# Kernel optimization log

Measured on AMD Instinct MI355X. Metric: run time of the kernel, lower is better.

## Reference

```python
import jax, jax.numpy as jnp
import numpy as np

H = 64          # hidden_size
IN = 6          # input_size
PREDICT = 10    # predict_size


def _lstm_cell(x_t, h, c, Wih, Whh, bih, bhh):
    # PyTorch gate order: i, f, g, o ; gates = x W_ih^T + b_ih + h W_hh^T + b_hh
    g = x_t @ Wih.T + bih + h @ Whh.T + bhh            # [B, 4H]
    i, f, gg, o = jnp.split(g, 4, axis=-1)
    c_new = jax.nn.sigmoid(f) * c + jax.nn.sigmoid(i) * jnp.tanh(gg)
    h_new = jax.nn.sigmoid(o) * jnp.tanh(c_new)
    return h_new, c_new


def setup_inputs() -> dict:
    key = jax.random.key(0)
    ks = jax.random.split(key, 12)
    B, T = 4096, 1024
    s = 1.0 / np.sqrt(H)  # torch default uniform init bound
    u = lambda k, shape: jax.random.uniform(k, shape, jnp.float32, -s, s)
    return {
        "x": jax.random.normal(ks[0], (B, T, IN), jnp.float32),
        "W_ih0": u(ks[1], (4 * H, IN)),
        "W_hh0": u(ks[2], (4 * H, H)),
        "b_ih0": u(ks[3], (4 * H,)),
        "b_hh0": u(ks[4], (4 * H,)),
        "W_ih1": u(ks[5], (4 * H, H)),
        "W_hh1": u(ks[6], (4 * H, H)),
        "b_ih1": u(ks[7], (4 * H,)),
        "b_hh1": u(ks[8], (4 * H,)),
        "fc_w": u(ks[9], (IN, H)),
        "fc_b": u(ks[10], (IN,)),
    }


def reference(x, W_ih0, W_hh0, b_ih0, b_hh0, W_ih1, W_hh1, b_ih1, b_hh1, fc_w, fc_b):
    B = x.shape[0]
    zeros = jnp.zeros((B, H), x.dtype)
    init = (zeros, zeros, zeros, zeros)  # h0, c0, h1, c1

    def stacked_step(carry, x_t):
        h0, c0, h1, c1 = carry
        h0, c0 = _lstm_cell(x_t, h0, c0, W_ih0, W_hh0, b_ih0, b_hh0)
        h1, c1 = _lstm_cell(h0, h1, c1, W_ih1, W_hh1, b_ih1, b_hh1)
        return (h0, c0, h1, c1), None

    # Encoder: scan over time (batch_first -> transpose to [T, B, IN])
    carry, _ = jax.lax.scan(stacked_step, init, jnp.swapaxes(x, 0, 1))

    def dec_step(state, _):
        dec_in, c = state
        c, _ = stacked_step(c, dec_in)
        pred = c[0 + 2] @ fc_w.T + fc_b  # top-layer h -> [B, IN]
        return (pred, c), pred

    dec_in0 = x[:, -1, :]
    _, preds = jax.lax.scan(dec_step, (dec_in0, carry), None, length=PREDICT)
    return jnp.swapaxes(preds, 0, 1)  # [B, PREDICT, IN]
```

## Files before the change

kernel.cpp:

```cpp
#include <hip/hip_runtime.h>

#define T_SEQ   1024
#define INDIM   6
#define HDIM    64
#define NPRED   10
#define CHNK    128
#define S0      104
#define NROWS   16

typedef __bf16         bf16x8 __attribute__((ext_vector_type(8)));
typedef float          f32x4  __attribute__((ext_vector_type(4)));
typedef unsigned short us4    __attribute__((ext_vector_type(4)));

#define MFMA16(a, b, c) __builtin_amdgcn_mfma_f32_16x16x32_bf16((a), (b), (c), 0, 0, 0)

static __device__ __forceinline__ float bf2f(unsigned short b) {
  union { unsigned int u; float f; } v; v.u = ((unsigned int)b) << 16; return v.f;
}
static __device__ __forceinline__ unsigned short f2bf(float f) {
  union { float f; unsigned int u; } v; v.f = f;
  unsigned int r = v.u + 0x7FFFu + ((v.u >> 16) & 1u);
  return (unsigned short)(r >> 16);
}

template <bool F32>
__global__ __launch_bounds__(512, 2)
void lstm2_pipe(const void* __restrict__ xv,
                const void* __restrict__ Wih0v,
                const void* __restrict__ Whh0v,
                const void* __restrict__ bih0v,
                const void* __restrict__ bhh0v,
                const void* __restrict__ Wih1v,
                const void* __restrict__ Whh1v,
                const void* __restrict__ bih1v,
                const void* __restrict__ bhh1v,
                const void* __restrict__ fcwv,
                const void* __restrict__ fcbv,
                void* __restrict__ outv)
{
  {
    const unsigned short* w0u = (const unsigned short*)Wih0v;
    int votes = 0;
#pragma unroll
    for (int i = 0; i < 16; ++i) {
      const unsigned e = (w0u[2 * i] >> 7) & 0xFF;
      votes += (e >= 0x80 || e <= 0x40) ? 1 : 0;
    }
    if ((votes >= 4) != F32) return;
  }

  __shared__ __align__(16) unsigned short A0[2][NROWS * S0];
  __shared__ __align__(16) unsigned short A1[2][NROWS * S0];
  __shared__ __align__(16) unsigned short XB[NROWS * CHNK * INDIM];
  __shared__ __align__(16) unsigned short FCW[INDIM * HDIM];
  __shared__ float FCB[INDIM];

  const int tid   = threadIdx.x;
  const int lane  = tid & 63;
  const int wave  = tid >> 6;
  const bool isA  = (wave < 4);
  const int  wv4  = wave & 3;
  const int  q    = lane >> 4;
  const int  n    = lane & 15;
  const int  u    = 16 * wv4 + n;
  const int rbase = blockIdx.x * NROWS;

  {
    unsigned short* p0 = &A0[0][0];
    unsigned short* p1 = &A1[0][0];
    for (int i = tid; i < 2 * NROWS * S0; i += 512) { p0[i] = 0; p1[i] = 0; }
  }
  for (int i = tid; i < INDIM * HDIM; i += 512) {
    if constexpr (F32) FCW[i] = f2bf(((const float*)fcwv)[i]);
    else               FCW[i] = ((const unsigned short*)fcwv)[i];
  }
  if (tid < INDIM) {
    if constexpr (F32) FCB[tid] = ((const float*)fcbv)[tid];
    else               FCB[tid] = bf2f(((const unsigned short*)fcbv)[tid]);
  }

  auto ld1 = [&](const void* p, int i) -> float {
    if constexpr (F32) return ((const float*)p)[i];
    else               return bf2f(((const unsigned short*)p)[i]);
  };
  auto ld8 = [&](const void* W, int off) -> bf16x8 {
    union { unsigned short us[8]; bf16x8 v; } t;
    if constexpr (F32) {
      const float* p = (const float*)W + off;
#pragma unroll
      for (int j = 0; j < 8; ++j) t.us[j] = f2bf(p[j]);
    } else {
      t.v = *(const bf16x8*)((const unsigned short*)W + off);
    }
    return t.v;
  };

  auto load_chunk = [&](int t0c) {
    if constexpr (F32) {
      const char* xb = (const char*)xv;
      for (int c = tid; c < NROWS * 192; c += 512) {
        const int row = c / 192;
        const int off = c - row * 192;
        const float4 v = *(const float4*)(xb + (size_t)(rbase + row) * (T_SEQ * INDIM * 4)
                                             + (size_t)t0c * (INDIM * 4) + (size_t)off * 16);
        us4 o;
        o.x = f2bf(v.x); o.y = f2bf(v.y); o.z = f2bf(v.z); o.w = f2bf(v.w);
        *(us4*)((char*)XB + (size_t)c * 8) = o;
      }
    } else {
      const char* xb = (const char*)xv;
      for (int c = tid; c < NROWS * 96; c += 512) {
        const int row = c / 96;
        const int off = c - row * 96;
        const int4 v = *(const int4*)(xb + (size_t)(rbase + row) * (T_SEQ * INDIM * 2)
                                         + (size_t)t0c * (INDIM * 2) + (size_t)off * 16);
        *(int4*)((char*)XB + (size_t)c * 16) = v;
      }
    }
  };

  load_chunk(0);
  __syncthreads();

  const int xrow   = tid / INDIM;
  const int xk     = tid - xrow * INDIM;
  const int xWrOff = xrow * S0 + HDIM + xk;
  const int xbBase = xrow * (CHNK * INDIM) + xk;

  if (tid < 96) A0[0][xWrOff] = XB[xbBase];
  __syncthreads();

  const int aOff  = n * S0 + 8 * q;
  const int hOffW = n * S0 + 16 * wv4 + 4 * q;
  const int bOff  = 16 * wv4 + 4 * q;

  float cc[4] = {0.f, 0.f, 0.f, 0.f};

  auto ldbias = [&](const void* b1, const void* b2, int gt) -> f32x4 {
    f32x4 r;
#pragma unroll
    for (int j = 0; j < 4; ++j)
      r[j] = ld1(b1, 64 * gt + bOff + j) + ld1(b2, 64 * gt + bOff + j);
    return r;
  };

  auto act4 = [&](const f32x4 gI, const f32x4 gF, const f32x4 gG, const f32x4 gO,
                  unsigned short* dst) {
    unsigned short hb[4];
#pragma unroll
    for (int r = 0; r < 4; ++r) {
      const float Ae = __builtin_amdgcn_exp2f(gF[r] * -1.442695040888963f);
      const float Be = __builtin_amdgcn_exp2f(gI[r] * -1.442695040888963f);
      const float Ge = __builtin_amdgcn_exp2f(gG[r] * -2.885390081777927f);
      const float M1 = (1.0f + Be) * (1.0f + Ge);
      const float nm = cc[r] * M1 + (1.0f - Ge) * (1.0f + Ae);
      cc[r] = nm * __builtin_amdgcn_rcpf((1.0f + Ae) * M1);
      const float Oe = __builtin_amdgcn_exp2f(gO[r] * -1.442695040888963f);
      const float Ee = __builtin_amdgcn_exp2f(cc[r] * -2.885390081777927f);
      hb[r] = f2bf((1.0f - Ee) * __builtin_amdgcn_rcpf((1.0f + Ee) * (1.0f + Oe)));
    }
    const unsigned int lo = (unsigned int)hb[0] | ((unsigned int)hb[1] << 16);
    const unsigned int hi = (unsigned int)hb[2] | ((unsigned int)hb[3] << 16);
    uint2 pk; pk.x = lo; pk.y = hi;
    *(uint2*)(dst + hOffW) = pk;
  };

  unsigned short* H0 = &A0[0][0];
  unsigned short* H1 = &A1[1][0];

  if (isA) {
    bf16x8 WA[12]; f32x4 bvA[4];
#pragma unroll
    for (int gt = 0; gt < 4; ++gt) {
      const int col = 64 * gt + u;
      WA[gt * 3 + 0] = ld8(Whh0v, col * HDIM + 8 * q);
      WA[gt * 3 + 1] = ld8(Whh0v, col * HDIM + 32 + 8 * q);
      union { unsigned short us[8]; bf16x8 v; } t2;
#pragma unroll
      for (int j = 0; j < 8; ++j) t2.us[j] = 0;
      if (q == 0) {
#pragma unroll
        for (int j = 0; j < INDIM; ++j) t2.us[j] = f2bf(ld1(Wih0v, col * INDIM + j));
      }
      WA[gt * 3 + 2] = t2.v;
      bvA[gt] = ldbias(bih0v, bhh0v, gt);
    }

    int t0v = 0;
    for (int i = 0; i <= T_SEQ; ++i) {
      if (((i + 1) & (CHNK - 1)) == 0 && (i + 1) < T_SEQ) {
        load_chunk(i + 1);
        __syncthreads();
        t0v = i + 1;
      }
      const int cur = i & 1;
      if (i < T_SEQ) {
        const unsigned short* A0c = &A0[cur][0];
        unsigned short*       A0n = &A0[cur ^ 1][0];
        const bf16x8 f0 = *(const bf16x8*)(A0c + aOff);
        const bf16x8 f1 = *(const bf16x8*)(A0c + aOff + 32);
        const bf16x8 f2 = *(const bf16x8*)(A0c + aOff + 64);
        f32x4 g0 = MFMA16(WA[0], f0, bvA[0]); g0 = MFMA16(WA[1],  f1, g0); g0 = MFMA16(WA[2],  f2, g0);
        f32x4 g1 = MFMA16(WA[3], f0, bvA[1]); g1 = MFMA16(WA[4],  f1, g1); g1 = MFMA16(WA[5],  f2, g1);
        f32x4 g2 = MFMA16(WA[6], f0, bvA[2]); g2 = MFMA16(WA[7],  f1, g2); g2 = MFMA16(WA[8],  f2, g2);
        f32x4 g3 = MFMA16(WA[9], f0, bvA[3]); g3 = MFMA16(WA[10], f1, g3); g3 = MFMA16(WA[11], f2, g3);
        act4(g0, g1, g2, g3, A0n);
        const int srct = (i + 1 < T_SEQ) ? (i + 1) : (T_SEQ - 1);
        if (tid < 96) A0n[xWrOff] = XB[xbBase + (srct - t0v) * INDIM];
      }
      __syncthreads();
    }
    for (int d = 0; d < NPRED; ++d) {
      const bf16x8 fa0 = *(const bf16x8*)(H0 + aOff);
      const bf16x8 fa1 = *(const bf16x8*)(H0 + aOff + 32);
      const bf16x8 fa2 = *(const bf16x8*)(H0 + aOff + 64);
      __syncthreads();
      {
        f32x4 g0 = MFMA16(WA[0], fa0, bvA[0]); g0 = MFMA16(WA[1],  fa1, g0); g0 = MFMA16(WA[2],  fa2, g0);
        f32x4 g1 = MFMA16(WA[3], fa0, bvA[1]); g1 = MFMA16(WA[4],  fa1, g1); g1 = MFMA16(WA[5],  fa2, g1);
        f32x4 g2 = MFMA16(WA[6], fa0, bvA[2]); g2 = MFMA16(WA[7],  fa1, g2); g2 = MFMA16(WA[8],  fa2, g2);
        f32x4 g3 = MFMA16(WA[9], fa0, bvA[3]); g3 = MFMA16(WA[10], fa1, g3); g3 = MFMA16(WA[11], fa2, g3);
        act4(g0, g1, g2, g3, H0);
      }
      __syncthreads();
      __syncthreads();
      if (tid < 96) {
        const unsigned short* h1row = H1 + xrow * S0;
        const int4* hp = (const int4*)h1row;
        const int4* wp = (const int4*)(&FCW[xk * HDIM]);
        float s = FCB[xk];
#pragma unroll
        for (int i8 = 0; i8 < 8; ++i8) {
          const int4 hv = hp[i8];
          const int4 wv2 = wp[i8];
          const unsigned int hu[4] = {(unsigned)hv.x, (unsigned)hv.y, (unsigned)hv.z, (unsigned)hv.w};
          const unsigned int wu[4] = {(unsigned)wv2.x, (unsigned)wv2.y, (unsigned)wv2.z, (unsigned)wv2.w};
#pragma unroll
          for (int k2 = 0; k2 < 4; ++k2) {
            union { unsigned int uu; float ff; } hl, hh2, wl, wh;
            hl.uu = hu[k2] << 16; hh2.uu = hu[k2] & 0xFFFF0000u;
            wl.uu = wu[k2] << 16; wh.uu  = wu[k2] & 0xFFFF0000u;
            s += hl.ff * wl.ff + hh2.ff * wh.ff;
          }
        }
        const unsigned short pb = f2bf(s);
        const size_t idx = (size_t)(rbase + xrow) * (NPRED * INDIM) + (size_t)d * INDIM + xk;
        if constexpr (F32) ((float*)outv)[idx] = s;
        else               ((unsigned short*)outv)[idx] = pb;
        H0[xWrOff] = pb;
      }
      __syncthreads();
    }
  } else {
    bf16x8 WB[16]; f32x4 bvB[4];
#pragma unroll
    for (int gt = 0; gt < 4; ++gt) {
      const int col = 64 * gt + u;
      WB[gt * 4 + 0] = ld8(Wih1v, col * HDIM + 8 * q);
      WB[gt * 4 + 1] = ld8(Wih1v, col * HDIM + 32 + 8 * q);
      WB[gt * 4 + 2] = ld8(Whh1v, col * HDIM + 8 * q);
      WB[gt * 4 + 3] = ld8(Whh1v, col * HDIM + 32 + 8 * q);
      bvB[gt] = ldbias(bih1v, bhh1v, gt);
    }

    for (int i = 0; i <= T_SEQ; ++i) {
      if (((i + 1) & (CHNK - 1)) == 0 && (i + 1) < T_SEQ) {
        load_chunk(i + 1);
        __syncthreads();
      }
      const int cur = i & 1;
      if (i >= 1) {
        const unsigned short* A0c = &A0[cur][0];
        const unsigned short* A1c = &A1[cur][0];
        unsigned short*       A1n = &A1[cur ^ 1][0];
        const bf16x8 h0a = *(const bf16x8*)(A0c + aOff);
        const bf16x8 h0b = *(const bf16x8*)(A0c + aOff + 32);
        const bf16x8 r0  = *(const bf16x8*)(A1c + aOff);
        const bf16x8 r1  = *(const bf16x8*)(A1c + aOff + 32);
        f32x4 g0 = MFMA16(WB[0],  h0a, bvB[0]); g0 = MFMA16(WB[1],  h0b, g0); g0 = MFMA16(WB[2],  r0, g0); g0 = MFMA16(WB[3],  r1, g0);
        f32x4 g1 = MFMA16(WB[4],  h0a, bvB[1]); g1 = MFMA16(WB[5],  h0b, g1); g1 = MFMA16(WB[6],  r0, g1); g1 = MFMA16(WB[7],  r1, g1);
        f32x4 g2 = MFMA16(WB[8],  h0a, bvB[2]); g2 = MFMA16(WB[9],  h0b, g2); g2 = MFMA16(WB[10], r0, g2); g2 = MFMA16(WB[11], r1, g2);
        f32x4 g3 = MFMA16(WB[12], h0a, bvB[3]); g3 = MFMA16(WB[13], h0b, g3); g3 = MFMA16(WB[14], r0, g3); g3 = MFMA16(WB[15], r1, g3);
        act4(g0, g1, g2, g3, A1n);
      }
      __syncthreads();
    }
    for (int d = 0; d < NPRED; ++d) {
      const bf16x8 fr0 = *(const bf16x8*)(H1 + aOff);
      const bf16x8 fr1 = *(const bf16x8*)(H1 + aOff + 32);
      __syncthreads();
      __syncthreads();
      {
        const bf16x8 h0a = *(const bf16x8*)(H0 + aOff);
        const bf16x8 h0b = *(const bf16x8*)(H0 + aOff + 32);
        f32x4 g0 = MFMA16(WB[0],  h0a, bvB[0]); g0 = MFMA16(WB[1],  h0b, g0); g0 = MFMA16(WB[2],  fr0, g0); g0 = MFMA16(WB[3],  fr1, g0);
        f32x4 g1 = MFMA16(WB[4],  h0a, bvB[1]); g1 = MFMA16(WB[5],  h0b, g1); g1 = MFMA16(WB[6],  fr0, g1); g1 = MFMA16(WB[7],  fr1, g1);
        f32x4 g2 = MFMA16(WB[8],  h0a, bvB[2]); g2 = MFMA16(WB[9],  h0b, g2); g2 = MFMA16(WB[10], fr0, g2); g2 = MFMA16(WB[11], fr1, g2);
        f32x4 g3 = MFMA16(WB[12], h0a, bvB[3]); g3 = MFMA16(WB[13], h0b, g3); g3 = MFMA16(WB[14], fr0, g3); g3 = MFMA16(WB[15], fr1, g3);
        act4(g0, g1, g2, g3, H1);
      }
      __syncthreads();
      __syncthreads();
    }
  }
}

extern "C" void kernel_launch(void* const* d_in, const int* in_sizes, int n_in,
                              void* d_out, int out_size, void* d_ws, size_t ws_size,
                              hipStream_t stream) {
  (void)in_sizes; (void)n_in; (void)d_ws; (void)ws_size; (void)out_size;
  const void* x    = d_in[0];
  const void* Wih0 = d_in[1];
  const void* Whh0 = d_in[2];
  const void* bih0 = d_in[3];
  const void* bhh0 = d_in[4];
  const void* Wih1 = d_in[5];
  const void* Whh1 = d_in[6];
  const void* bih1 = d_in[7];
  const void* bhh1 = d_in[8];
  const void* fcw  = d_in[9];
  const void* fcb  = d_in[10];
  lstm2_pipe<true><<<dim3(4096 / NROWS), dim3(512), 0, stream>>>(
      x, Wih0, Whh0, bih0, bhh0, Wih1, Whh1, bih1, bhh1, fcw, fcb, d_out);
  lstm2_pipe<false><<<dim3(4096 / NROWS), dim3(512), 0, stream>>>(
      x, Wih0, Whh0, bih0, bhh0, Wih1, Whh1, bih1, bhh1, fcw, fcb, d_out);
}
```

Before: 921.0 us.

## Replace block barriers with LDS flag counters between layer-0 and layer-1 waves

Replaces the per-timestep __syncthreads between the layer-0 producer waves and the layer-1 consumer waves with LDS counter flags (atomic bumps plus spin-wait with s_sleep). Layer-0 h is kept in a 4-deep ring buffer so layer 0 can run up to three steps ahead of layer 1. The x-chunk loads are now done only by the layer-0 waves. The aim is to decouple the two layers and remove lockstep barrier stalls. It adds spin-polling overhead and relies on memory ordering from the volatile LDS flags and block-scope fences.

New measurement: 963.7 us. 4.6% more time.

```diff
diff --git a/kernel.cpp b/kernel.cpp
--- a/kernel.cpp
+++ b/kernel.cpp
@@ -25,7 +25,7 @@
 
 template <bool F32>
 __global__ __launch_bounds__(512, 2)
-void lstm2_pipe(const void* __restrict__ xv,
+void lstm2_flag(const void* __restrict__ xv,
                 const void* __restrict__ Wih0v,
                 const void* __restrict__ Whh0v,
                 const void* __restrict__ bih0v,
@@ -49,11 +49,12 @@
     if ((votes >= 4) != F32) return;
   }
 
-  __shared__ __align__(16) unsigned short A0[2][NROWS * S0];
-  __shared__ __align__(16) unsigned short A1[2][NROWS * S0];
+  __shared__ __align__(16) unsigned short A0r[4][NROWS * S0];
+  __shared__ __align__(16) unsigned short A1r[2][NROWS * S0];
   __shared__ __align__(16) unsigned short XB[NROWS * CHNK * INDIM];
   __shared__ __align__(16) unsigned short FCW[INDIM * HDIM];
   __shared__ float FCB[INDIM];
+  __shared__ int SY[8];
 
   const int tid   = threadIdx.x;
   const int lane  = tid & 63;
@@ -66,9 +67,11 @@
   const int rbase = blockIdx.x * NROWS;
 
   {
-    unsigned short* p0 = &A0[0][0];
-    unsigned short* p1 = &A1[0][0];
-    for (int i = tid; i < 2 * NROWS * S0; i += 512) { p0[i] = 0; p1[i] = 0; }
+    unsigned short* p0 = &A0r[0][0];
+    for (int i = tid; i < 4 * NROWS * S0; i += 512) p0[i] = 0;
+    unsigned short* p1 = &A1r[0][0];
+    for (int i = tid; i < 2 * NROWS * S0; i += 512) p1[i] = 0;
+    if (tid < 8) SY[tid] = 0;
   }
   for (int i = tid; i < INDIM * HDIM; i += 512) {
     if constexpr (F32) FCW[i] = f2bf(((const float*)fcwv)[i]);
@@ -98,7 +101,7 @@
   auto load_chunk = [&](int t0c) {
     if constexpr (F32) {
       const char* xb = (const char*)xv;
-      for (int c = tid; c < NROWS * 192; c += 512) {
+      for (int c = tid; c < NROWS * 192; c += 256) {
         const int row = c / 192;
         const int off = c - row * 192;
         const float4 v = *(const float4*)(xb + (size_t)(rbase + row) * (T_SEQ * INDIM * 4)
@@ -109,7 +112,7 @@
       }
     } else {
       const char* xb = (const char*)xv;
-      for (int c = tid; c < NROWS * 96; c += 512) {
+      for (int c = tid; c < NROWS * 96; c += 256) {
         const int row = c / 96;
         const int off = c - row * 96;
         const int4 v = *(const int4*)(xb + (size_t)(rbase + row) * (T_SEQ * INDIM * 2)
@@ -119,7 +122,17 @@
     }
   };
 
-  load_chunk(0);
+  volatile int* vSY = SY;
+  auto waitge = [&](int idx, int tgt) {
+    while (vSY[idx] < tgt) __builtin_amdgcn_s_sleep(1);
+    __threadfence_block();
+  };
+  auto bump = [&](int idx) {
+    __threadfence_block();
+    if (lane == 0) atomicAdd(&SY[idx], 1);
+  };
+
+  if (isA) load_chunk(0);
   __syncthreads();
 
   const int xrow   = tid / INDIM;
@@ -127,7 +140,7 @@
   const int xWrOff = xrow * S0 + HDIM + xk;
   const int xbBase = xrow * (CHNK * INDIM) + xk;
 
-  if (tid < 96) A0[0][xWrOff] = XB[xbBase];
+  if (tid < 96) A0r[3][xWrOff] = XB[xbBase];
   __syncthreads();
 
   const int aOff  = n * S0 + 8 * q;
@@ -165,8 +178,8 @@
     *(uint2*)(dst + hOffW) = pk;
   };
 
-  unsigned short* H0 = &A0[0][0];
-  unsigned short* H1 = &A1[1][0];
+  unsigned short* H0 = &A0r[3][0];
+  unsigned short* H1 = &A1r[1][0];
 
   if (isA) {
     bf16x8 WA[12]; f32x4 bvA[4];
@@ -187,29 +200,31 @@
     }
 
     int t0v = 0;
-    for (int i = 0; i <= T_SEQ; ++i) {
+    for (int i = 0; i < T_SEQ; ++i) {
+      waitge(0, 4 * i);
+      if (i >= 3) waitge(1, 4 * (i - 3));
       if (((i + 1) & (CHNK - 1)) == 0 && (i + 1) < T_SEQ) {
         load_chunk(i + 1);
-        __syncthreads();
+        bump(2);
+        waitge(2, 4 * ((i + 1) >> 7));
         t0v = i + 1;
       }
-      const int cur = i & 1;
-      if (i < T_SEQ) {
-        const unsigned short* A0c = &A0[cur][0];
-        unsigned short*       A0n = &A0[cur ^ 1][0];
-        const bf16x8 f0 = *(const bf16x8*)(A0c + aOff);
-        const bf16x8 f1 = *(const bf16x8*)(A0c + aOff + 32);
-        const bf16x8 f2 = *(const bf16x8*)(A0c + aOff + 64);
-        f32x4 g0 = MFMA16(WA[0], f0, bvA[0]); g0 = MFMA16(WA[1],  f1, g0); g0 = MFMA16(WA[2],  f2, g0);
-        f32x4 g1 = MFMA16(WA[3], f0, bvA[1]); g1 = MFMA16(WA[4],  f1, g1); g1 = MFMA16(WA[5],  f2, g1);
-        f32x4 g2 = MFMA16(WA[6], f0, bvA[2]); g2 = MFMA16(WA[7],  f1, g2); g2 = MFMA16(WA[8],  f2, g2);
-        f32x4 g3 = MFMA16(WA[9], f0, bvA[3]); g3 = MFMA16(WA[10], f1, g3); g3 = MFMA16(WA[11], f2, g3);
-        act4(g0, g1, g2, g3, A0n);
-        const int srct = (i + 1 < T_SEQ) ? (i + 1) : (T_SEQ - 1);
-        if (tid < 96) A0n[xWrOff] = XB[xbBase + (srct - t0v) * INDIM];
-      }
-      __syncthreads();
-    }
+      const unsigned short* A0c = &A0r[(i + 3) & 3][0];
+      unsigned short*       A0n = &A0r[i & 3][0];
+      const bf16x8 f0 = *(const bf16x8*)(A0c + aOff);
+      const bf16x8 f1 = *(const bf16x8*)(A0c + aOff + 32);
+      const bf16x8 f2 = *(const bf16x8*)(A0c + aOff + 64);
+      f32x4 g0 = MFMA16(WA[0], f0, bvA[0]); g0 = MFMA16(WA[1],  f1, g0); g0 = MFMA16(WA[2],  f2, g0);
+      f32x4 g1 = MFMA16(WA[3], f0, bvA[1]); g1 = MFMA16(WA[4],  f1, g1); g1 = MFMA16(WA[5],  f2, g1);
+      f32x4 g2 = MFMA16(WA[6], f0, bvA[2]); g2 = MFMA16(WA[7],  f1, g2); g2 = MFMA16(WA[8],  f2, g2);
+      f32x4 g3 = MFMA16(WA[9], f0, bvA[3]); g3 = MFMA16(WA[10], f1, g3); g3 = MFMA16(WA[11], f2, g3);
+      act4(g0, g1, g2, g3, A0n);
+      const int srct = (i + 1 < T_SEQ) ? (i + 1) : (T_SEQ - 1);
+      if (tid < 96) A0n[xWrOff] = XB[xbBase + (srct - t0v) * INDIM];
+      bump(0);
+    }
+    waitge(1, 4 * T_SEQ);
+
     for (int d = 0; d < NPRED; ++d) {
       const bf16x8 fa0 = *(const bf16x8*)(H0 + aOff);
       const bf16x8 fa1 = *(const bf16x8*)(H0 + aOff + 32);
@@ -263,28 +278,24 @@
       bvB[gt] = ldbias(bih1v, bhh1v, gt);
     }
 
-    for (int i = 0; i <= T_SEQ; ++i) {
-      if (((i + 1) & (CHNK - 1)) == 0 && (i + 1) < T_SEQ) {
-        load_chunk(i + 1);
-        __syncthreads();
-      }
-      const int cur = i & 1;
-      if (i >= 1) {
-        const unsigned short* A0c = &A0[cur][0];
-        const unsigned short* A1c = &A1[cur][0];
-        unsigned short*       A1n = &A1[cur ^ 1][0];
-        const bf16x8 h0a = *(const bf16x8*)(A0c + aOff);
-        const bf16x8 h0b = *(const bf16x8*)(A0c + aOff + 32);
-        const bf16x8 r0  = *(const bf16x8*)(A1c + aOff);
-        const bf16x8 r1  = *(const bf16x8*)(A1c + aOff + 32);
-        f32x4 g0 = MFMA16(WB[0],  h0a, bvB[0]); g0 = MFMA16(WB[1],  h0b, g0); g0 = MFMA16(WB[2],  r0, g0); g0 = MFMA16(WB[3],  r1, g0);
-        f32x4 g1 = MFMA16(WB[4],  h0a, bvB[1]); g1 = MFMA16(WB[5],  h0b, g1); g1 = MFMA16(WB[6],  r0, g1); g1 = MFMA16(WB[7],  r1, g1);
-        f32x4 g2 = MFMA16(WB[8],  h0a, bvB[2]); g2 = MFMA16(WB[9],  h0b, g2); g2 = MFMA16(WB[10], r0, g2); g2 = MFMA16(WB[11], r1, g2);
-        f32x4 g3 = MFMA16(WB[12], h0a, bvB[3]); g3 = MFMA16(WB[13], h0b, g3); g3 = MFMA16(WB[14], r0, g3); g3 = MFMA16(WB[15], r1, g3);
-        act4(g0, g1, g2, g3, A1n);
-      }
-      __syncthreads();
-    }
+    for (int k = 0; k < T_SEQ; ++k) {
+      waitge(0, 4 * (k + 1));
+      waitge(1, 4 * k);
+      const unsigned short* A0c = &A0r[k & 3][0];
+      const unsigned short* A1c = &A1r[(k + 1) & 1][0];
+      unsigned short*       A1n = &A1r[k & 1][0];
+      const bf16x8 h0a = *(const bf16x8*)(A0c + aOff);
+      const bf16x8 h0b = *(const bf16x8*)(A0c + aOff + 32);
+      const bf16x8 r0  = *(const bf16x8*)(A1c + aOff);
+      const bf16x8 r1  = *(const bf16x8*)(A1c + aOff + 32);
+      f32x4 g0 = MFMA16(WB[0],  h0a, bvB[0]); g0 = MFMA16(WB[1],  h0b, g0); g0 = MFMA16(WB[2],  r0, g0); g0 = MFMA16(WB[3],  r1, g0);
+      f32x4 g1 = MFMA16(WB[4],  h0a, bvB[1]); g1 = MFMA16(WB[5],  h0b, g1); g1 = MFMA16(WB[6],  r0, g1); g1 = MFMA16(WB[7],  r1, g1);
+      f32x4 g2 = MFMA16(WB[8],  h0a, bvB[2]); g2 = MFMA16(WB[9],  h0b, g2); g2 = MFMA16(WB[10], r0, g2); g2 = MFMA16(WB[11], r1, g2);
+      f32x4 g3 = MFMA16(WB[12], h0a, bvB[3]); g3 = MFMA16(WB[13], h0b, g3); g3 = MFMA16(WB[14], r0, g3); g3 = MFMA16(WB[15], r1, g3);
+      act4(g0, g1, g2, g3, A1n);
+      bump(1);
+    }
+
     for (int d = 0; d < NPRED; ++d) {
       const bf16x8 fr0 = *(const bf16x8*)(H1 + aOff);
       const bf16x8 fr1 = *(const bf16x8*)(H1 + aOff + 32);
@@ -320,8 +331,8 @@
   const void* bhh1 = d_in[8];
   const void* fcw  = d_in[9];
   const void* fcb  = d_in[10];
-  lstm2_pipe<true><<<dim3(4096 / NROWS), dim3(512), 0, stream>>>(
+  lstm2_flag<true><<<dim3(4096 / NROWS), dim3(512), 0, stream>>>(
       x, Wih0, Whh0, bih0, bhh0, Wih1, Whh1, bih1, bhh1, fcw, fcb, d_out);
-  lstm2_pipe<false><<<dim3(4096 / NROWS), dim3(512), 0, stream>>>(
+  lstm2_flag<false><<<dim3(4096 / NROWS), dim3(512), 0, stream>>>(
       x, Wih0, Whh0, bih0, bhh0, Wih1, Whh1, bih1, bhh1, fcw, fcb, d_out);
 }
```
